# Optimization experiments

Measured on AMD Instinct MI355X. Metric: run time of the kernel, lower is better.

The kernel has to match this reference:

```python
import jax, jax.numpy as jnp
import numpy as np

N_NODES, N_EDGES, D_IN, D_HID, D_OUT = 100000, 3200000, 512, 64, 64


def _gcn_conv(x, W, b, src, dst, n_nodes):
    """PyG-style GCNConv: x' = D^{-1/2} A_hat D^{-1/2} (x W) + b, self-loops already in (src,dst)."""
    h = x @ W  # [N, F_out]
    deg = jax.ops.segment_sum(jnp.ones_like(dst, dtype=h.dtype), dst, num_segments=n_nodes)
    dinv = jax.lax.rsqrt(deg)  # deg >= 1 because self-loops are included
    norm = dinv[src] * dinv[dst]  # [E]
    msg = h[src] * norm[:, None]  # gather + scale, [E, F_out]
    return jax.ops.segment_sum(msg, dst, num_segments=n_nodes) + b


def setup_inputs() -> dict:
    key = jax.random.key(0)
    ks = jax.random.split(key, 8)
    x = jax.random.normal(ks[0], (N_NODES, D_IN), dtype=jnp.float32)
    edge_index = jax.random.randint(ks[1], (2, N_EDGES), 0, N_NODES, dtype=jnp.int32)
    W1 = jax.random.normal(ks[2], (D_IN, D_HID), dtype=jnp.float32) * (1.0 / np.sqrt(D_IN))
    b1 = jnp.zeros((D_HID,), dtype=jnp.float32)
    W2 = jax.random.normal(ks[3], (D_HID, D_OUT), dtype=jnp.float32) * (1.0 / np.sqrt(D_HID))
    b2 = jnp.zeros((D_OUT,), dtype=jnp.float32)
    Wlin = jax.random.normal(ks[4], (D_HID, D_OUT), dtype=jnp.float32) * (1.0 / np.sqrt(D_HID))
    blin = jnp.zeros((D_OUT,), dtype=jnp.float32)
    return {"x": x, "edge_index": edge_index, "W1": W1, "b1": b1,
            "W2": W2, "b2": b2, "Wlin": Wlin, "blin": blin}


def reference(x, edge_index, W1, b1, W2, b2, Wlin, blin):
    n = x.shape[0]
    loops = jnp.arange(n, dtype=edge_index.dtype)
    src = jnp.concatenate([edge_index[0], loops])
    dst = jnp.concatenate([edge_index[1], loops])
    h = _gcn_conv(x, W1, b1, src, dst, n)
    h = jax.nn.relu(h)
    h = _gcn_conv(h, W2, b2, src, dst, n)
    return h @ Wlin + blin
```

## Files before the change

### kernel.cpp

```cpp
#include <hip/hip_runtime.h>

#define DIN 512
#define DH  64
#define BKT_SHIFT 10
#define BKT_NODES 1024
#define MAXBKT 128
#define TILE 8192
#define SRC_BITS 17
#define SRC_MASK ((1u << SRC_BITS) - 1)

typedef __attribute__((ext_vector_type(8))) _Float16 half8_t;
typedef __attribute__((ext_vector_type(4))) float float4_t;

__global__ __launch_bounds__(256) void k_prepbin(const float* __restrict__ W1,
                                                 const float* __restrict__ W2,
                                                 const float* __restrict__ b2,
                                                 const float* __restrict__ Wlin,
                                                 const float* __restrict__ blin,
                                                 _Float16* __restrict__ Wt,
                                                 _Float16* __restrict__ Wct,
                                                 float* __restrict__ bias_out,
                                                 const int* __restrict__ src,
                                                 const int* __restrict__ dst,
                                                 int n_edges,
                                                 int* __restrict__ gcur,
                                                 unsigned int* __restrict__ tmp,
                                                 int nbkt, int cap) {
  const int tid = threadIdx.x;
  if (blockIdx.x == 0) {
    __shared__ float WcS[64 * 64];
    for (int idx = tid; idx < 64 * 64; idx += 256) {
      int i = idx >> 6, j = idx & 63;
      float s = 0.f;
      #pragma unroll 8
      for (int k = 0; k < 64; ++k) s = fmaf(W2[i * 64 + k], Wlin[k * 64 + j], s);
      WcS[idx] = s;
    }
    if (tid < 64) {
      float s = blin[tid];
      #pragma unroll 8
      for (int k = 0; k < 64; ++k) s = fmaf(b2[k], Wlin[k * 64 + tid], s);
      bias_out[tid] = s;
    }
    __syncthreads();
    for (int G = tid; G < 64 * 64 / 8; G += 256) {
      int n = G >> 3, k = (G & 7) * 8;
      half8_t h;
      #pragma unroll
      for (int j = 0; j < 8; ++j) h[j] = (_Float16)WcS[(k + j) * 64 + n];
      *(half8_t*)&Wct[(size_t)n * 64 + k] = h;
    }
  } else if (blockIdx.x <= 4) {
    __shared__ _Float16 T[64][136];
    const int k0 = (blockIdx.x - 1) * 128;
    for (int idx = tid; idx < 128 * 64; idx += 256) {
      int kk = idx >> 6, n = idx & 63;
      T[n][kk] = (_Float16)W1[(size_t)(k0 + kk) * 64 + n];
    }
    __syncthreads();
    for (int G = tid; G < 64 * 16; G += 256) {
      int n = G >> 4, g = (G & 15) * 8;
      half8_t h = *(const half8_t*)&T[n][g];
      *(half8_t*)&Wt[(size_t)n * 512 + k0 + g] = h;
    }
  } else {
    __shared__ int cnt[MAXBKT];
    __shared__ int base[MAXBKT];
    for (int b = tid; b < nbkt; b += 256) cnt[b] = 0;
    __syncthreads();
    int e0 = (blockIdx.x - 5) * TILE;
    int e1 = min(e0 + TILE, n_edges);
    for (int e = e0 + tid; e < e1; e += 256)
      atomicAdd(&cnt[dst[e] >> BKT_SHIFT], 1);
    __syncthreads();
    for (int b = tid; b < nbkt; b += 256) {
      int c = cnt[b];
      base[b] = c ? (b * cap + atomicAdd(&gcur[b], c)) : 0;
      cnt[b] = 0;
    }
    __syncthreads();
    for (int e = e0 + tid; e < e1; e += 256) {
      int d = dst[e];
      int bkt = d >> BKT_SHIFT;
      int off = atomicAdd(&cnt[bkt], 1);
      int pos = base[bkt] + off;
      if (pos < (bkt + 1) * cap)
        tmp[pos] = (unsigned int)src[e] |
                   ((unsigned int)(d & (BKT_NODES - 1)) << SRC_BITS);
    }
  }
}

__global__ __launch_bounds__(256) void k_place(const unsigned int* __restrict__ tmp,
                                               const int* __restrict__ gcur,
                                               int* __restrict__ rowbeg,
                                               int* __restrict__ rowcnt,
                                               float* __restrict__ dinv,
                                               int* __restrict__ srcs,
                                               int n_nodes, int cap) {
  __shared__ int cnt[BKT_NODES];
  __shared__ int sh[256];
  const int t = threadIdx.x;
  const int bkt = blockIdx.x;
  #pragma unroll
  for (int k = 0; k < BKT_NODES / 256; ++k) cnt[t + 256 * k] = 0;
  __syncthreads();
  const int beg = bkt * cap;
  const int end = beg + min(gcur[bkt], cap);
  for (int j = beg + t; j < end; j += 256)
    atomicAdd(&cnt[tmp[j] >> SRC_BITS], 1);
  __syncthreads();
  int v[4];
  int s = 0;
  const int base = t * 4;
  #pragma unroll
  for (int k = 0; k < 4; ++k) {
    v[k] = cnt[base + k];
    s += v[k];
  }
  sh[t] = s;
  __syncthreads();
  for (int off = 1; off < 256; off <<= 1) {
    int x = sh[t];
    int y = (t >= off) ? sh[t - off] : 0;
    __syncthreads();
    sh[t] = x + y;
    __syncthreads();
  }
  int excl = sh[t] - s;
  #pragma unroll
  for (int k = 0; k < 4; ++k) {
    int idx = base + k;
    int node = (bkt << BKT_SHIFT) + idx;
    if (node < n_nodes) {
      rowbeg[node] = beg + excl;
      rowcnt[node] = v[k];
      dinv[node] = rsqrtf((float)(v[k] + 1));
    }
    cnt[idx] = excl;
    excl += v[k];
  }
  __syncthreads();
  for (int j = beg + t; j < end; j += 256) {
    unsigned int e = tmp[j];
    int r = e >> SRC_BITS;
    int pos = atomicAdd(&cnt[r], 1);
    srcs[beg + pos] = (int)(e & SRC_MASK);
  }
}

template <int KDIM, bool A_HALF>
__global__ __launch_bounds__(1024) void k_mfma(const void* __restrict__ Ain,
                                               const _Float16* __restrict__ Bt,
                                               const float* __restrict__ dinv,
                                               _Float16* __restrict__ Ch, int M) {
  constexpr int BS_HALVES = (64 * KDIM > 16384) ? 64 * KDIM : 16384;
  __shared__ _Float16 Bs[BS_HALVES];
  const int tid = threadIdx.x;
  for (int G = tid; G < 8 * KDIM; G += 1024) {
    int n = G / (KDIM / 8);
    int g = G % (KDIM / 8);
    half8_t h = *(const half8_t*)&Bt[(size_t)G * 8];
    *(half8_t*)&Bs[n * KDIM + ((g ^ (n & 7)) * 8)] = h;
  }
  __syncthreads();

  const int wave = tid >> 6, lane = tid & 63;
  const int quad = lane >> 4, lrow = lane & 15;
  const int row = blockIdx.x * 256 + wave * 16 + lrow;
  const int rowc = min(row, M - 1);

  float4_t acc[4] = {{0.f, 0.f, 0.f, 0.f}, {0.f, 0.f, 0.f, 0.f},
                     {0.f, 0.f, 0.f, 0.f}, {0.f, 0.f, 0.f, 0.f}};

  #pragma unroll
  for (int k0 = 0; k0 < KDIM; k0 += 32) {
    half8_t a;
    if (A_HALF) {
      a = *(const half8_t*)((const _Float16*)Ain + (size_t)rowc * KDIM + k0 + quad * 8);
    } else {
      const float* Af = (const float*)Ain + (size_t)rowc * KDIM + k0 + quad * 8;
      float4 x0 = *(const float4*)Af;
      float4 x1 = *(const float4*)(Af + 4);
      a[0] = (_Float16)x0.x; a[1] = (_Float16)x0.y;
      a[2] = (_Float16)x0.z; a[3] = (_Float16)x0.w;
      a[4] = (_Float16)x1.x; a[5] = (_Float16)x1.y;
      a[6] = (_Float16)x1.z; a[7] = (_Float16)x1.w;
    }
    const int g = (k0 >> 3) + quad;
    #pragma unroll
    for (int nb = 0; nb < 4; ++nb) {
      int n = nb * 16 + lrow;
      half8_t b = *(const half8_t*)&Bs[n * KDIM + ((g ^ (n & 7)) * 8)];
      acc[nb] = __builtin_amdgcn_mfma_f32_16x16x32_f16(a, b, acc[nb], 0, 0, 0);
    }
  }

  const int orow_base = blockIdx.x * 256 + wave * 16 + quad * 4;
  float dnr[4];
  #pragma unroll
  for (int r = 0; r < 4; ++r) dnr[r] = dinv[min(orow_base + r, M - 1)];

  __syncthreads();
  _Float16* scratch = Bs + wave * 1024;
  #pragma unroll
  for (int nb = 0; nb < 4; ++nb)
    #pragma unroll
    for (int r = 0; r < 4; ++r)
      scratch[(quad * 4 + r) * 64 + nb * 16 + lrow] = (_Float16)(acc[nb][r] * dnr[r]);
  const int r2 = lane >> 2, c2 = (lane & 3) * 16;
  const int row_out = blockIdx.x * 256 + wave * 16 + r2;
  half8_t o0 = *(const half8_t*)&scratch[r2 * 64 + c2];
  half8_t o1 = *(const half8_t*)&scratch[r2 * 64 + c2 + 8];
  if (row_out < M) {
    *(half8_t*)&Ch[(size_t)row_out * 64 + c2] = o0;
    *(half8_t*)&Ch[(size_t)row_out * 64 + c2 + 8] = o1;
  }
}

__global__ __launch_bounds__(256) void k_gather(const _Float16* __restrict__ fs,
                                                const int* __restrict__ rowbeg,
                                                const int* __restrict__ rowcnt,
                                                const int* __restrict__ srcs,
                                                const float* __restrict__ dinv,
                                                const float* __restrict__ bias,
                                                _Float16* __restrict__ outh,
                                                float* __restrict__ outf,
                                                int n_nodes) {
  int node = blockIdx.x * 4 + (threadIdx.x >> 6);
  int lane = threadIdx.x & 63;
  if (node >= n_nodes) return;
  const int esub = lane >> 3;
  const int ch8 = (lane & 7) * 8;
  const int beg = rowbeg[node];
  const int end = beg + rowcnt[node];
  float acc[8] = {0.f, 0.f, 0.f, 0.f, 0.f, 0.f, 0.f, 0.f};
  int j = beg;
  for (; j + 16 <= end; j += 16) {
    int s0 = srcs[j + esub];
    int s1 = srcs[j + 8 + esub];
    half8_t f0 = *(const half8_t*)&fs[(size_t)s0 * 64 + ch8];
    half8_t f1 = *(const half8_t*)&fs[(size_t)s1 * 64 + ch8];
    #pragma unroll
    for (int k = 0; k < 8; ++k) acc[k] += (float)f0[k];
    #pragma unroll
    for (int k = 0; k < 8; ++k) acc[k] += (float)f1[k];
  }
  for (; j < end; j += 8) {
    int idx = j + esub;
    bool act = idx < end;
    int s = srcs[act ? idx : beg];
    float w = act ? 1.f : 0.f;
    half8_t f = *(const half8_t*)&fs[(size_t)s * 64 + ch8];
    #pragma unroll
    for (int k = 0; k < 8; ++k) acc[k] = fmaf((float)f[k], w, acc[k]);
  }
  #pragma unroll
  for (int m = 8; m <= 32; m <<= 1)
    #pragma unroll
    for (int k = 0; k < 8; ++k) acc[k] += __shfl_xor(acc[k], m, 64);
  if (esub == 0) {
    float dn = dinv[node];
    half8_t sf = *(const half8_t*)&fs[(size_t)node * 64 + ch8];
    float v[8];
    #pragma unroll
    for (int k = 0; k < 8; ++k)
      v[k] = fmaf(acc[k] + (float)sf[k], dn, bias[ch8 + k]);
    if (outh) {
      half8_t o;
      #pragma unroll
      for (int k = 0; k < 8; ++k) o[k] = (_Float16)fmaxf(v[k], 0.f);
      *(half8_t*)&outh[(size_t)node * 64 + ch8] = o;
    } else {
      float4 o0 = make_float4(v[0], v[1], v[2], v[3]);
      float4 o1 = make_float4(v[4], v[5], v[6], v[7]);
      *(float4*)&outf[(size_t)node * 64 + ch8] = o0;
      *(float4*)&outf[(size_t)node * 64 + ch8 + 4] = o1;
    }
  }
}

extern "C" void kernel_launch(void* const* d_in, const int* in_sizes, int n_in,
                              void* d_out, int out_size, void* d_ws, size_t ws_size,
                              hipStream_t stream) {
  const float* x    = (const float*)d_in[0];
  const int*   ei   = (const int*)d_in[1];
  const float* W1   = (const float*)d_in[2];
  const float* b1   = (const float*)d_in[3];
  const float* W2   = (const float*)d_in[4];
  const float* b2   = (const float*)d_in[5];
  const float* Wlin = (const float*)d_in[6];
  const float* blin = (const float*)d_in[7];
  float* out = (float*)d_out;

  const int n_nodes = in_sizes[0] / DIN;
  const int n_edges = in_sizes[1] / 2;
  const int* src = ei;
  const int* dst = ei + n_edges;
  const int nbkt = (n_nodes + BKT_NODES - 1) >> BKT_SHIFT;
  const int ntiles = (n_edges + TILE - 1) / TILE;
  const int cap = ((n_edges / nbkt) * 5 / 4 + 1024 + 255) & ~255;

  char* ws = (char*)d_ws;
  size_t off = 0;
  auto alloc = [&](size_t bytes) {
    void* p = ws + off;
    off += (bytes + 255) & ~(size_t)255;
    return p;
  };
  const size_t featH = (size_t)n_nodes * DH * 2;
  const size_t padE = (size_t)nbkt * cap;
  _Float16*     fs1      = (_Float16*)alloc(featH);
  _Float16*     h1r      = (_Float16*)alloc(featH);
  _Float16*     fs2      = (_Float16*)alloc(featH);
  unsigned int* tmp      = (unsigned int*)alloc(padE * 4);
  int*          srcs     = (int*)alloc(padE * 4);
  float*        dinv     = (float*)alloc((size_t)n_nodes * 4);
  int*          rowbeg   = (int*)alloc((size_t)n_nodes * 4);
  int*          rowcnt   = (int*)alloc((size_t)n_nodes * 4);
  int*          gcur     = (int*)alloc((size_t)MAXBKT * 4);
  _Float16*     Wt       = (_Float16*)alloc(64 * 512 * 2);
  _Float16*     Wct      = (_Float16*)alloc(64 * 64 * 2);
  float*        bias_out = (float*)alloc(64 * 4);

  hipMemsetAsync(gcur, 0, (size_t)nbkt * 4, stream);

  k_prepbin<<<5 + ntiles, 256, 0, stream>>>(W1, W2, b2, Wlin, blin, Wt, Wct,
                                            bias_out, src, dst, n_edges, gcur,
                                            tmp, nbkt, cap);
  k_place<<<nbkt, 256, 0, stream>>>(tmp, gcur, rowbeg, rowcnt, dinv, srcs,
                                    n_nodes, cap);

  const int mblocks = (n_nodes + 255) / 256;
  const int agblocks = (n_nodes + 3) / 4;

  k_mfma<512, false><<<mblocks, 1024, 0, stream>>>(x, Wt, dinv, fs1, n_nodes);
  k_gather<<<agblocks, 256, 0, stream>>>(fs1, rowbeg, rowcnt, srcs, dinv, b1,
                                         h1r, nullptr, n_nodes);

  k_mfma<64, true><<<mblocks, 1024, 0, stream>>>(h1r, Wct, dinv, fs2, n_nodes);
  k_gather<<<agblocks, 256, 0, stream>>>(fs2, rowbeg, rowcnt, srcs, dinv,
                                         bias_out, nullptr, out, n_nodes);
}
```

Before: 571.7 us.

## Split gather features into four 16-channel planes for cache-local passes

The MFMA epilogue now writes its fp16 output as four column planes of 16 channels each (a [4][N][16] layout) instead of row-major [N][64]. The gather kernel runs a 2D grid with one plane per blockIdx.y, and each wave now covers 32 edges times 2 channel groups per step. Each pass touches a working set a quarter of the size (about 3.2 MB per plane), so random neighbour gathers are more likely to hit in L2/MALL. In exchange, the edge index lists and rowbeg/rowcnt are re-read four times, and each gather loads only 32-byte rows, which lowers bytes per memory transaction.

```diff
diff --git a/kernel.cpp b/kernel.cpp
--- a/kernel.cpp
+++ b/kernel.cpp
@@ -213,8 +213,9 @@
   half8_t o0 = *(const half8_t*)&scratch[r2 * 64 + c2];
   half8_t o1 = *(const half8_t*)&scratch[r2 * 64 + c2 + 8];
   if (row_out < M) {
-    *(half8_t*)&Ch[(size_t)row_out * 64 + c2] = o0;
-    *(half8_t*)&Ch[(size_t)row_out * 64 + c2 + 8] = o1;
+    _Float16* d0 = Ch + ((size_t)(c2 >> 4) * M + row_out) * 16;
+    *(half8_t*)d0 = o0;
+    *(half8_t*)(d0 + 8) = o1;
   }
 }
 
@@ -230,52 +231,54 @@
   int node = blockIdx.x * 4 + (threadIdx.x >> 6);
   int lane = threadIdx.x & 63;
   if (node >= n_nodes) return;
-  const int esub = lane >> 3;
-  const int ch8 = (lane & 7) * 8;
+  const int pass = blockIdx.y;
+  const int esub = lane >> 1;
+  const int cg = (lane & 1) * 8;
+  const _Float16* ft = fs + (size_t)pass * n_nodes * 16;
   const int beg = rowbeg[node];
   const int end = beg + rowcnt[node];
   float acc[8] = {0.f, 0.f, 0.f, 0.f, 0.f, 0.f, 0.f, 0.f};
   int j = beg;
-  for (; j + 16 <= end; j += 16) {
+  for (; j + 64 <= end; j += 64) {
     int s0 = srcs[j + esub];
-    int s1 = srcs[j + 8 + esub];
-    half8_t f0 = *(const half8_t*)&fs[(size_t)s0 * 64 + ch8];
-    half8_t f1 = *(const half8_t*)&fs[(size_t)s1 * 64 + ch8];
+    int s1 = srcs[j + 32 + esub];
+    half8_t f0 = *(const half8_t*)&ft[(size_t)s0 * 16 + cg];
+    half8_t f1 = *(const half8_t*)&ft[(size_t)s1 * 16 + cg];
     #pragma unroll
     for (int k = 0; k < 8; ++k) acc[k] += (float)f0[k];
     #pragma unroll
     for (int k = 0; k < 8; ++k) acc[k] += (float)f1[k];
   }
-  for (; j < end; j += 8) {
+  for (; j < end; j += 32) {
     int idx = j + esub;
     bool act = idx < end;
     int s = srcs[act ? idx : beg];
     float w = act ? 1.f : 0.f;
-    half8_t f = *(const half8_t*)&fs[(size_t)s * 64 + ch8];
+    half8_t f = *(const half8_t*)&ft[(size_t)s * 16 + cg];
     #pragma unroll
     for (int k = 0; k < 8; ++k) acc[k] = fmaf((float)f[k], w, acc[k]);
   }
   #pragma unroll
-  for (int m = 8; m <= 32; m <<= 1)
+  for (int m = 2; m <= 32; m <<= 1)
     #pragma unroll
     for (int k = 0; k < 8; ++k) acc[k] += __shfl_xor(acc[k], m, 64);
   if (esub == 0) {
     float dn = dinv[node];
-    half8_t sf = *(const half8_t*)&fs[(size_t)node * 64 + ch8];
+    half8_t sf = *(const half8_t*)&ft[(size_t)node * 16 + cg];
     float v[8];
     #pragma unroll
     for (int k = 0; k < 8; ++k)
-      v[k] = fmaf(acc[k] + (float)sf[k], dn, bias[ch8 + k]);
+      v[k] = fmaf(acc[k] + (float)sf[k], dn, bias[pass * 16 + cg + k]);
     if (outh) {
       half8_t o;
       #pragma unroll
       for (int k = 0; k < 8; ++k) o[k] = (_Float16)fmaxf(v[k], 0.f);
-      *(half8_t*)&outh[(size_t)node * 64 + ch8] = o;
+      *(half8_t*)&outh[(size_t)node * 64 + pass * 16 + cg] = o;
     } else {
       float4 o0 = make_float4(v[0], v[1], v[2], v[3]);
       float4 o1 = make_float4(v[4], v[5], v[6], v[7]);
-      *(float4*)&outf[(size_t)node * 64 + ch8] = o0;
-      *(float4*)&outf[(size_t)node * 64 + ch8 + 4] = o1;
+      *(float4*)&outf[(size_t)node * 64 + pass * 16 + cg] = o0;
+      *(float4*)&outf[(size_t)node * 64 + pass * 16 + cg + 4] = o1;
     }
   }
 }
@@ -332,13 +335,13 @@
                                     n_nodes, cap);
 
   const int mblocks = (n_nodes + 255) / 256;
-  const int agblocks = (n_nodes + 3) / 4;
+  const dim3 gg((n_nodes + 3) / 4, 4);
 
   k_mfma<512, false><<<mblocks, 1024, 0, stream>>>(x, Wt, dinv, fs1, n_nodes);
-  k_gather<<<agblocks, 256, 0, stream>>>(fs1, rowbeg, rowcnt, srcs, dinv, b1,
-                                         h1r, nullptr, n_nodes);
+  k_gather<<<gg, 256, 0, stream>>>(fs1, rowbeg, rowcnt, srcs, dinv, b1,
+                                   h1r, nullptr, n_nodes);
 
   k_mfma<64, true><<<mblocks, 1024, 0, stream>>>(h1r, Wct, dinv, fs2, n_nodes);
-  k_gather<<<agblocks, 256, 0, stream>>>(fs2, rowbeg, rowcnt, srcs, dinv,
-                                         bias_out, nullptr, out, n_nodes);
-}
+  k_gather<<<gg, 256, 0, stream>>>(fs2, rowbeg, rowcnt, srcs, dinv,
+                                   bias_out, nullptr, out, n_nodes);
+}
```

Measured after the change: 790.0 us. 38.2% more time.
